# Optimization experiments

Hardware: AMD Instinct MI355X
Metric: run time of the kernel (lower is better)

Reference implementation:

```python
import jax, jax.numpy as jnp
import numpy as np

N_NODES = 100000
N_EDGES = 1600000
D_IN = 128
D_OUT = 128


def setup_inputs() -> dict:
    key = jax.random.key(0)
    ks = jax.random.split(key, 7)
    x = jax.random.normal(ks[0], (N_NODES, D_IN), dtype=jnp.float32)
    h0 = jax.random.normal(ks[1], (N_NODES, D_IN), dtype=jnp.float32)
    adj_val = jax.random.uniform(ks[2], (N_EDGES,), dtype=jnp.float32)
    adj_src = jax.random.randint(ks[3], (N_EDGES,), 0, N_NODES, dtype=jnp.int32)
    adj_dst = jax.random.randint(ks[4], (N_EDGES,), 0, N_NODES, dtype=jnp.int32)
    stdv = 1.0 / np.sqrt(D_OUT)
    weight = jax.random.uniform(ks[5], (D_IN, D_OUT), dtype=jnp.float32, minval=-stdv, maxval=stdv)
    weight_r = jax.random.uniform(ks[6], (D_IN, D_OUT), dtype=jnp.float32, minval=-stdv, maxval=stdv)
    return {"x": x, "h0": h0, "adj_val": adj_val, "weight": weight,
            "weight_r": weight_r, "adj_src": adj_src, "adj_dst": adj_dst}


def reference(x, h0, adj_val, weight, weight_r, adj_src, adj_dst):
    # hi = spmm(adj, x): COO sparse matmul as weighted gather + segment-sum.
    msgs = adj_val[:, None] * x[adj_src]              # [E, D_IN]
    hi = jax.ops.segment_sum(msgs, adj_dst, num_segments=x.shape[0])  # [N, D_IN]
    # variant=False: no concat with h0. residual=True: + x @ weight_r.
    out = hi @ weight + x @ weight_r                   # [N, D_OUT]
    return out
```

## Files before the change

### kernel.cpp

```cpp
#include <hip/hip_runtime.h>
#include <hip/hip_fp16.h>


typedef __attribute__((ext_vector_type(8))) short bf16x8;
typedef __attribute__((ext_vector_type(4))) float f32x4;

#define BSH 8
#define CHUNK 4096
#define K2 18

__device__ __forceinline__ unsigned short f2b(float f) {
    unsigned u = __float_as_uint(f);
    return (unsigned short)((u + 0x7FFFu + ((u >> 16) & 1u)) >> 16);
}

__global__ __launch_bounds__(256) void wprep(const float* __restrict__ W,
                                             const float* __restrict__ Wr,
                                             unsigned short* __restrict__ Wt,
                                             unsigned short* __restrict__ Wrt,
                                             int* __restrict__ ccnt,
                                             int NBK) {
    int gid = blockIdx.x * 256 + threadIdx.x;
    if (gid < 16384) {
        int k = gid >> 7, n = gid & 127;
        Wt[(n << 7) + k]  = f2b(W[gid]);
        Wrt[(n << 7) + k] = f2b(Wr[gid]);
    }
    if (gid < NBK) ccnt[gid] = 0;
}

__global__ __launch_bounds__(512) void gemm_mfma(const float* __restrict__ x,
                                                 const unsigned short* __restrict__ Wt,
                                                 const unsigned short* __restrict__ Wrt,
                                                 unsigned* __restrict__ z8u,
                                                 float* __restrict__ rowscale,
                                                 float* __restrict__ out, int N) {
    __shared__ uint4 lw[4096];
    const int tid = threadIdx.x;
    const int wave = tid >> 6;
    const int lane = tid & 63;
    const int l15 = lane & 15;
    const int lhi = lane >> 4;

    const uint4* wtg = reinterpret_cast<const uint4*>(Wt);
    const uint4* wrg = reinterpret_cast<const uint4*>(Wrt);
    #pragma unroll
    for (int it = 0; it < 4; ++it) {
        int c = it * 512 + tid;
        int row = c >> 4, cc = c & 15;
        int sc = cc ^ (row & 7);
        lw[row * 16 + sc] = wtg[c];
        lw[2048 + row * 16 + sc] = wrg[c];
    }
    __syncthreads();

    const int rowBase = blockIdx.x * 256 + wave * 32;
    const int r0 = rowBase + l15;
    const int r1 = rowBase + 16 + l15;
    const size_t xo0 = (size_t)(r0 < N ? r0 : N - 1) * 128;
    const size_t xo1 = (size_t)(r1 < N ? r1 : N - 1) * 128;

    f32x4 accW[8][2], accR[8][2];
    #pragma unroll
    for (int fn = 0; fn < 8; ++fn) {
        accW[fn][0] = (f32x4)0.f; accW[fn][1] = (f32x4)0.f;
        accR[fn][0] = (f32x4)0.f; accR[fn][1] = (f32x4)0.f;
    }

    #pragma unroll
    for (int ks = 0; ks < 4; ++ks) {
        const int kb = ks * 32 + lhi * 8;
        float4 a0 = *reinterpret_cast<const float4*>(&x[xo0 + kb]);
        float4 b0 = *reinterpret_cast<const float4*>(&x[xo0 + kb + 4]);
        float4 a1 = *reinterpret_cast<const float4*>(&x[xo1 + kb]);
        float4 b1 = *reinterpret_cast<const float4*>(&x[xo1 + kb + 4]);
        union { bf16x8 v; unsigned u[4]; } xf0, xf1;
        xf0.u[0] = (unsigned)f2b(a0.x) | ((unsigned)f2b(a0.y) << 16);
        xf0.u[1] = (unsigned)f2b(a0.z) | ((unsigned)f2b(a0.w) << 16);
        xf0.u[2] = (unsigned)f2b(b0.x) | ((unsigned)f2b(b0.y) << 16);
        xf0.u[3] = (unsigned)f2b(b0.z) | ((unsigned)f2b(b0.w) << 16);
        xf1.u[0] = (unsigned)f2b(a1.x) | ((unsigned)f2b(a1.y) << 16);
        xf1.u[1] = (unsigned)f2b(a1.z) | ((unsigned)f2b(a1.w) << 16);
        xf1.u[2] = (unsigned)f2b(b1.x) | ((unsigned)f2b(b1.y) << 16);
        xf1.u[3] = (unsigned)f2b(b1.z) | ((unsigned)f2b(b1.w) << 16);

        const int sl = ks * 4 + lhi;
        #pragma unroll
        for (int fn = 0; fn < 8; ++fn) {
            int wrow = fn * 16 + l15;
            int idx = wrow * 16 + (sl ^ (wrow & 7));
            bf16x8 wf  = *reinterpret_cast<const bf16x8*>(&lw[idx]);
            bf16x8 wrf = *reinterpret_cast<const bf16x8*>(&lw[2048 + idx]);
            accW[fn][0] = __builtin_amdgcn_mfma_f32_16x16x32_bf16(wf,  xf0.v, accW[fn][0], 0, 0, 0);
            accW[fn][1] = __builtin_amdgcn_mfma_f32_16x16x32_bf16(wf,  xf1.v, accW[fn][1], 0, 0, 0);
            accR[fn][0] = __builtin_amdgcn_mfma_f32_16x16x32_bf16(wrf, xf0.v, accR[fn][0], 0, 0, 0);
            accR[fn][1] = __builtin_amdgcn_mfma_f32_16x16x32_bf16(wrf, xf1.v, accR[fn][1], 0, 0, 0);
        }
    }

    #pragma unroll
    for (int fr = 0; fr < 2; ++fr) {
        int row = rowBase + fr * 16 + l15;
        float m = 0.f;
        #pragma unroll
        for (int fn = 0; fn < 8; ++fn)
            #pragma unroll
            for (int j = 0; j < 4; ++j)
                m = fmaxf(m, fabsf(accW[fn][fr][j]));
        m = fmaxf(m, __shfl_xor(m, 16));
        m = fmaxf(m, __shfl_xor(m, 32));
        m = fmaxf(m, 1e-20f);
        const float qs = 127.0f / m;

        if (row >= N) continue;
        if (lhi == 0) rowscale[row] = m * (1.0f / 127.0f);
        #pragma unroll
        for (int fn = 0; fn < 8; ++fn) {
            int c = fn * 16 + lhi * 4;
            *reinterpret_cast<f32x4*>(&out[(size_t)row * 128 + c]) = accR[fn][fr];
            int q0 = (int)rintf(accW[fn][fr][0] * qs);
            int q1 = (int)rintf(accW[fn][fr][1] * qs);
            int q2 = (int)rintf(accW[fn][fr][2] * qs);
            int q3 = (int)rintf(accW[fn][fr][3] * qs);
            unsigned pq = (unsigned)(q0 & 255) | ((unsigned)(q1 & 255) << 8) |
                          ((unsigned)(q2 & 255) << 16) | ((unsigned)(q3 & 255) << 24);
            z8u[(size_t)row * 32 + fn * 4 + lhi] = pq;
        }
    }
}

__global__ __launch_bounds__(256) void histc(const int* __restrict__ dst,
                                             int* __restrict__ ccnt, int E, int NBK) {
    __shared__ int lh[512];
    for (int i = threadIdx.x; i < NBK; i += 256) lh[i] = 0;
    __syncthreads();
    const int base = blockIdx.x * CHUNK;
    #pragma unroll
    for (int i = 0; i < CHUNK / 256; ++i) {
        int e = base + i * 256 + threadIdx.x;
        if (e < E) atomicAdd(&lh[dst[e] >> BSH], 1);
    }
    __syncthreads();
    for (int i = threadIdx.x; i < NBK; i += 256)
        if (lh[i]) atomicAdd(&ccnt[i], lh[i]);
}

__global__ __launch_bounds__(256) void scanc(const int* __restrict__ ccnt, int* __restrict__ coff,
                                             int* __restrict__ ccur, int NBK) {
    __shared__ int sh[256];
    const int t = threadIdx.x;
    const int i0 = t * 2;
    int c0 = (i0 < NBK) ? ccnt[i0] : 0;
    int c1 = (i0 + 1 < NBK) ? ccnt[i0 + 1] : 0;
    int s = c0 + c1;
    sh[t] = s;
    __syncthreads();
    #pragma unroll
    for (int d = 1; d < 256; d <<= 1) {
        int v = (t >= d) ? sh[t - d] : 0;
        __syncthreads();
        sh[t] += v;
        __syncthreads();
    }
    int ex = sh[t] - s;
    if (i0 < NBK) { coff[i0] = ex; ccur[i0] = ex; }
    if (i0 + 1 < NBK) { coff[i0 + 1] = ex + c0; ccur[i0 + 1] = ex + c0; }
}

__global__ __launch_bounds__(256) void binsort1(const float* __restrict__ val,
                                                const int* __restrict__ src,
                                                const int* __restrict__ dst,
                                                int* __restrict__ ccur,
                                                uint2* __restrict__ epk1, int E, int NBK) {
    __shared__ int lh[512];
    __shared__ int lbase[512];
    for (int i = threadIdx.x; i < NBK; i += 256) lh[i] = 0;
    __syncthreads();
    const int base = blockIdx.x * CHUNK;
    int rank[CHUNK / 256];
    int bk[CHUNK / 256];
    #pragma unroll
    for (int i = 0; i < CHUNK / 256; ++i) {
        int e = base + i * 256 + threadIdx.x;
        if (e < E) {
            int b = dst[e] >> BSH;
            bk[i] = b;
            rank[i] = atomicAdd(&lh[b], 1);
        } else bk[i] = -1;
    }
    __syncthreads();
    for (int i = threadIdx.x; i < NBK; i += 256)
        lbase[i] = lh[i] ? atomicAdd(&ccur[i], lh[i]) : 0;
    __syncthreads();
    #pragma unroll
    for (int i = 0; i < CHUNK / 256; ++i) {
        int e = base + i * 256 + threadIdx.x;
        if (e >= E) break;
        int p = lbase[bk[i]] + rank[i];
        __half hv = __float2half(val[e]);
        unsigned short hu;
        __builtin_memcpy(&hu, &hv, 2);
        epk1[p] = make_uint2((unsigned)src[e] | ((unsigned)(hu & 0x7FFFu) << 17),
                             (unsigned)dst[e]);
    }
}

__global__ __launch_bounds__(256) void binsort2(const uint2* __restrict__ epk1,
                                                const int* __restrict__ coff,
                                                const int* __restrict__ ccnt,
                                                unsigned* __restrict__ epk,
                                                int* __restrict__ off,
                                                int* __restrict__ cnt, int N) {
    __shared__ int lcnt[256];
    __shared__ int sh[256];
    __shared__ int lcur[256];
    const int b = blockIdx.x;
    const int s = coff[b];
    const int n = ccnt[b];
    const int t = threadIdx.x;
    const int gnode = (b << BSH) + t;

    lcnt[t] = 0;
    __syncthreads();

    uint2 q[K2];
    #pragma unroll
    for (int r = 0; r < K2; ++r) {
        int i = t + r * 256;
        if (i < n) {
            q[r] = epk1[s + i];
            atomicAdd(&lcnt[q[r].y & 255], 1);
        }
    }
    for (int i = t + K2 * 256; i < n; i += 256)
        atomicAdd(&lcnt[epk1[s + i].y & 255], 1);
    __syncthreads();

    int c = lcnt[t];
    sh[t] = c;
    __syncthreads();
    #pragma unroll
    for (int d = 1; d < 256; d <<= 1) {
        int v = (t >= d) ? sh[t - d] : 0;
        __syncthreads();
        sh[t] += v;
        __syncthreads();
    }
    int ex = sh[t] - c;
    lcur[t] = ex;
    if (gnode < N) {
        off[gnode] = s + ex;
        cnt[gnode] = c;
    }
    __syncthreads();

    #pragma unroll
    for (int r = 0; r < K2; ++r) {
        int i = t + r * 256;
        if (i < n) {
            int p = s + atomicAdd(&lcur[q[r].y & 255], 1);
            epk[p] = ((q[r].x & 0x1FFFFu) << 15) | (q[r].x >> 17);
        }
    }
    for (int i = t + K2 * 256; i < n; i += 256) {
        uint2 v = epk1[s + i];
        int p = s + atomicAdd(&lcur[v.y & 255], 1);
        epk[p] = ((v.x & 0x1FFFFu) << 15) | (v.x >> 17);
    }
}

__device__ __forceinline__ float h15f(unsigned h) {
    unsigned short u = (unsigned short)(h & 0x7FFFu);
    __half hv;
    __builtin_memcpy(&hv, &u, 2);
    return __half2float(hv);
}

__global__ __launch_bounds__(256) void spmm_gather(const unsigned short* __restrict__ z8u,
                                                   const float* __restrict__ rowscale,
                                                   const unsigned* __restrict__ epk,
                                                   const int* __restrict__ off,
                                                   const int* __restrict__ cnt,
                                                   float* __restrict__ out, int N) {
    const int lane = threadIdx.x & 63;
    const int node = (int)((blockIdx.x * (size_t)blockDim.x + threadIdx.x) >> 6);
    if (node >= N) return;
    const int base = off[node];
    const int deg = cnt[node];
    float2 acc = *reinterpret_cast<const float2*>(&out[(size_t)node * 128 + lane * 2]);

    for (int b = 0; b < deg; b += 64) {
        int m = min(64, deg - b);
        unsigned pv = (lane < m) ? epk[base + b + lane] : 0u;
        int j = 0;
        for (; j + 4 <= m; j += 4) {
            unsigned p0 = __shfl(pv, j + 0);
            unsigned p1 = __shfl(pv, j + 1);
            unsigned p2 = __shfl(pv, j + 2);
            unsigned p3 = __shfl(pv, j + 3);
            unsigned s0 = p0 >> 15, s1 = p1 >> 15, s2 = p2 >> 15, s3 = p3 >> 15;
            unsigned short w0 = z8u[(size_t)s0 * 64 + lane];
            unsigned short w1 = z8u[(size_t)s1 * 64 + lane];
            unsigned short w2 = z8u[(size_t)s2 * 64 + lane];
            unsigned short w3 = z8u[(size_t)s3 * 64 + lane];
            float v0 = h15f(p0) * rowscale[s0];
            float v1 = h15f(p1) * rowscale[s1];
            float v2 = h15f(p2) * rowscale[s2];
            float v3 = h15f(p3) * rowscale[s3];
            acc.x = fmaf(v0, (float)(signed char)(w0 & 0xFF), acc.x);
            acc.y = fmaf(v0, (float)(signed char)(w0 >> 8), acc.y);
            acc.x = fmaf(v1, (float)(signed char)(w1 & 0xFF), acc.x);
            acc.y = fmaf(v1, (float)(signed char)(w1 >> 8), acc.y);
            acc.x = fmaf(v2, (float)(signed char)(w2 & 0xFF), acc.x);
            acc.y = fmaf(v2, (float)(signed char)(w2 >> 8), acc.y);
            acc.x = fmaf(v3, (float)(signed char)(w3 & 0xFF), acc.x);
            acc.y = fmaf(v3, (float)(signed char)(w3 >> 8), acc.y);
        }
        for (; j < m; ++j) {
            unsigned p = __shfl(pv, j);
            unsigned s = p >> 15;
            unsigned short wv = z8u[(size_t)s * 64 + lane];
            float v = h15f(p) * rowscale[s];
            acc.x = fmaf(v, (float)(signed char)(wv & 0xFF), acc.x);
            acc.y = fmaf(v, (float)(signed char)(wv >> 8), acc.y);
        }
    }
    *reinterpret_cast<float2*>(&out[(size_t)node * 128 + lane * 2]) = acc;
}

extern "C" void kernel_launch(void* const* d_in, const int* in_sizes, int n_in,
                              void* d_out, int out_size, void* d_ws, size_t ws_size,
                              hipStream_t stream) {
    const float* x    = (const float*)d_in[0];
    const float* aval = (const float*)d_in[2];
    const float* W    = (const float*)d_in[3];
    const float* Wr   = (const float*)d_in[4];
    const int*   asrc = (const int*)d_in[5];
    const int*   adst = (const int*)d_in[6];
    float* out = (float*)d_out;

    const int nx = in_sizes[0];
    const int N = nx / 128;
    const int E = in_sizes[2];
    const int NBK = (N + (1 << BSH) - 1) >> BSH;
    const int NB1 = (E + CHUNK - 1) / CHUNK;

    char* w = (char*)d_ws;
    uint2* epk1 = (uint2*)w;                  w += (size_t)E * 8;
    unsigned* z8 = (unsigned*)w;              w += (size_t)nx;
    float* rowscale = (float*)w;              w += (size_t)N * 4;
    unsigned short* Wt = (unsigned short*)w;  w += 16384 * 2;
    unsigned short* Wrt= (unsigned short*)w;  w += 16384 * 2;
    int* off    = (int*)w;  w += (size_t)N * 4;
    int* cnt    = (int*)w;  w += (size_t)N * 4;
    int* ccnt   = (int*)w;  w += 2048;
    int* coff   = (int*)w;  w += 2048;
    int* ccur   = (int*)w;  w += 2048;
    unsigned* epk = (unsigned*)w;  w += (size_t)E * 4;

    wprep<<<(16384 + 255) / 256, 256, 0, stream>>>(W, Wr, Wt, Wrt, ccnt, NBK);
    gemm_mfma<<<(N + 255) / 256, 512, 0, stream>>>(x, Wt, Wrt, z8, rowscale, out, N);
    histc<<<NB1, 256, 0, stream>>>(adst, ccnt, E, NBK);
    scanc<<<1, 256, 0, stream>>>(ccnt, coff, ccur, NBK);
    binsort1<<<NB1, 256, 0, stream>>>(aval, asrc, adst, ccur, epk1, E, NBK);
    binsort2<<<NBK, 256, 0, stream>>>(epk1, coff, ccnt, epk, off, cnt, N);
    spmm_gather<<<(int)(((size_t)N * 64 + 255) / 256), 256, 0, stream>>>(
        (const unsigned short*)z8, rowscale, epk, off, cnt, out, N);
}
```

Baseline: 150.3 us.

## Fold row scale into edge weights during sort and use scalar edge loads in gather

Edge weights are now multiplied by the per-source row scale in binsort2 and stored as a truncated bf16 in the packed edge word. That removes the random rowscale gather and the fp16 decode from the spmm inner loop. The gather kernel also drops the lane-load-plus-shuffle pattern, making offset and degree wave-uniform and reading packed edges directly as uniform loads. This should cut per-edge memory traffic and instructions in the hot loop, at the cost of precision, since bf16 with the sign bit dropped has fewer mantissa bits than fp16, plus extra random reads moved into the sort kernel.

```diff
diff --git a/kernel.cpp b/kernel.cpp
--- a/kernel.cpp
+++ b/kernel.cpp
@@ -205,9 +205,17 @@
     }
 }
 
+__device__ __forceinline__ float h15f(unsigned h) {
+    unsigned short u = (unsigned short)(h & 0x7FFFu);
+    __half hv;
+    __builtin_memcpy(&hv, &u, 2);
+    return __half2float(hv);
+}
+
 __global__ __launch_bounds__(256) void binsort2(const uint2* __restrict__ epk1,
                                                 const int* __restrict__ coff,
                                                 const int* __restrict__ ccnt,
+                                                const float* __restrict__ rowscale,
                                                 unsigned* __restrict__ epk,
                                                 int* __restrict__ off,
                                                 int* __restrict__ cnt, int N) {
@@ -258,26 +266,22 @@
     for (int r = 0; r < K2; ++r) {
         int i = t + r * 256;
         if (i < n) {
+            unsigned srcv = q[r].x & 0x1FFFFu;
+            float v = h15f(q[r].x >> 17) * rowscale[srcv];
             int p = s + atomicAdd(&lcur[q[r].y & 255], 1);
-            epk[p] = ((q[r].x & 0x1FFFFu) << 15) | (q[r].x >> 17);
+            epk[p] = (srcv << 15) | ((unsigned)f2b(v) & 0x7FFFu);
         }
     }
     for (int i = t + K2 * 256; i < n; i += 256) {
-        uint2 v = epk1[s + i];
-        int p = s + atomicAdd(&lcur[v.y & 255], 1);
-        epk[p] = ((v.x & 0x1FFFFu) << 15) | (v.x >> 17);
-    }
-}
-
-__device__ __forceinline__ float h15f(unsigned h) {
-    unsigned short u = (unsigned short)(h & 0x7FFFu);
-    __half hv;
-    __builtin_memcpy(&hv, &u, 2);
-    return __half2float(hv);
+        uint2 v2 = epk1[s + i];
+        unsigned srcv = v2.x & 0x1FFFFu;
+        float v = h15f(v2.x >> 17) * rowscale[srcv];
+        int p = s + atomicAdd(&lcur[v2.y & 255], 1);
+        epk[p] = (srcv << 15) | ((unsigned)f2b(v) & 0x7FFFu);
+    }
 }
 
 __global__ __launch_bounds__(256) void spmm_gather(const unsigned short* __restrict__ z8u,
-                                                   const float* __restrict__ rowscale,
                                                    const unsigned* __restrict__ epk,
                                                    const int* __restrict__ off,
                                                    const int* __restrict__ cnt,
@@ -285,45 +289,41 @@
     const int lane = threadIdx.x & 63;
     const int node = (int)((blockIdx.x * (size_t)blockDim.x + threadIdx.x) >> 6);
     if (node >= N) return;
-    const int base = off[node];
-    const int deg = cnt[node];
+    const int base = __builtin_amdgcn_readfirstlane(off[node]);
+    const int deg  = __builtin_amdgcn_readfirstlane(cnt[node]);
+    const unsigned* __restrict__ ep = epk + base;
+
     float2 acc = *reinterpret_cast<const float2*>(&out[(size_t)node * 128 + lane * 2]);
 
-    for (int b = 0; b < deg; b += 64) {
-        int m = min(64, deg - b);
-        unsigned pv = (lane < m) ? epk[base + b + lane] : 0u;
-        int j = 0;
-        for (; j + 4 <= m; j += 4) {
-            unsigned p0 = __shfl(pv, j + 0);
-            unsigned p1 = __shfl(pv, j + 1);
-            unsigned p2 = __shfl(pv, j + 2);
-            unsigned p3 = __shfl(pv, j + 3);
-            unsigned s0 = p0 >> 15, s1 = p1 >> 15, s2 = p2 >> 15, s3 = p3 >> 15;
-            unsigned short w0 = z8u[(size_t)s0 * 64 + lane];
-            unsigned short w1 = z8u[(size_t)s1 * 64 + lane];
-            unsigned short w2 = z8u[(size_t)s2 * 64 + lane];
-            unsigned short w3 = z8u[(size_t)s3 * 64 + lane];
-            float v0 = h15f(p0) * rowscale[s0];
-            float v1 = h15f(p1) * rowscale[s1];
-            float v2 = h15f(p2) * rowscale[s2];
-            float v3 = h15f(p3) * rowscale[s3];
-            acc.x = fmaf(v0, (float)(signed char)(w0 & 0xFF), acc.x);
-            acc.y = fmaf(v0, (float)(signed char)(w0 >> 8), acc.y);
-            acc.x = fmaf(v1, (float)(signed char)(w1 & 0xFF), acc.x);
-            acc.y = fmaf(v1, (float)(signed char)(w1 >> 8), acc.y);
-            acc.x = fmaf(v2, (float)(signed char)(w2 & 0xFF), acc.x);
-            acc.y = fmaf(v2, (float)(signed char)(w2 >> 8), acc.y);
-            acc.x = fmaf(v3, (float)(signed char)(w3 & 0xFF), acc.x);
-            acc.y = fmaf(v3, (float)(signed char)(w3 >> 8), acc.y);
-        }
-        for (; j < m; ++j) {
-            unsigned p = __shfl(pv, j);
-            unsigned s = p >> 15;
-            unsigned short wv = z8u[(size_t)s * 64 + lane];
-            float v = h15f(p) * rowscale[s];
-            acc.x = fmaf(v, (float)(signed char)(wv & 0xFF), acc.x);
-            acc.y = fmaf(v, (float)(signed char)(wv >> 8), acc.y);
-        }
+    int j = 0;
+    for (; j + 4 <= deg; j += 4) {
+        unsigned p0 = ep[j + 0];
+        unsigned p1 = ep[j + 1];
+        unsigned p2 = ep[j + 2];
+        unsigned p3 = ep[j + 3];
+        unsigned short w0 = z8u[(size_t)(p0 >> 15) * 64 + lane];
+        unsigned short w1 = z8u[(size_t)(p1 >> 15) * 64 + lane];
+        unsigned short w2 = z8u[(size_t)(p2 >> 15) * 64 + lane];
+        unsigned short w3 = z8u[(size_t)(p3 >> 15) * 64 + lane];
+        float v0 = __uint_as_float((p0 & 0x7FFFu) << 16);
+        float v1 = __uint_as_float((p1 & 0x7FFFu) << 16);
+        float v2 = __uint_as_float((p2 & 0x7FFFu) << 16);
+        float v3 = __uint_as_float((p3 & 0x7FFFu) << 16);
+        acc.x = fmaf(v0, (float)(signed char)(w0 & 0xFF), acc.x);
+        acc.y = fmaf(v0, (float)(signed char)(w0 >> 8), acc.y);
+        acc.x = fmaf(v1, (float)(signed char)(w1 & 0xFF), acc.x);
+        acc.y = fmaf(v1, (float)(signed char)(w1 >> 8), acc.y);
+        acc.x = fmaf(v2, (float)(signed char)(w2 & 0xFF), acc.x);
+        acc.y = fmaf(v2, (float)(signed char)(w2 >> 8), acc.y);
+        acc.x = fmaf(v3, (float)(signed char)(w3 & 0xFF), acc.x);
+        acc.y = fmaf(v3, (float)(signed char)(w3 >> 8), acc.y);
+    }
+    for (; j < deg; ++j) {
+        unsigned p = ep[j];
+        unsigned short wv = z8u[(size_t)(p >> 15) * 64 + lane];
+        float v = __uint_as_float((p & 0x7FFFu) << 16);
+        acc.x = fmaf(v, (float)(signed char)(wv & 0xFF), acc.x);
+        acc.y = fmaf(v, (float)(signed char)(wv >> 8), acc.y);
     }
     *reinterpret_cast<float2*>(&out[(size_t)node * 128 + lane * 2]) = acc;
 }
@@ -363,7 +363,7 @@
     histc<<<NB1, 256, 0, stream>>>(adst, ccnt, E, NBK);
     scanc<<<1, 256, 0, stream>>>(ccnt, coff, ccur, NBK);
     binsort1<<<NB1, 256, 0, stream>>>(aval, asrc, adst, ccur, epk1, E, NBK);
-    binsort2<<<NBK, 256, 0, stream>>>(epk1, coff, ccnt, epk, off, cnt, N);
+    binsort2<<<NBK, 256, 0, stream>>>(epk1, coff, ccnt, rowscale, epk, off, cnt, N);
     spmm_gather<<<(int)(((size_t)N * 64 + 255) / 256), 256, 0, stream>>>(
-        (const unsigned short*)z8, rowscale, epk, off, cnt, out, N);
-}
+        (const unsigned short*)z8, epk, off, cnt, out, N);
+}
```

Result: faster. 146.9 us (-2.2%).
